# Optimization experiments

Hardware: AMD Instinct MI355X
Metric: run time of the kernel (lower is better)

Reference implementation:

```python
import jax, jax.numpy as jnp
import numpy as np

VJ = 80      # vjointnum (groups)
FS = 480     # feature_size = 2*k of RFF
HD = 256     # hidden_dim
K = 240      # RFF k
BATCH = 2048
TWO_PI = 2.0 * np.pi
SLOPE = 0.01  # LeakyReLU default negative_slope


def _wn(v, g):
    # weight_norm (dim=0): w[o,:] = g[o] * v[o,:] / ||v[o,:]||
    return v * (g[:, None] / jnp.linalg.norm(v, axis=1, keepdims=True))


def _grouped(x, v, g, b):
    # x: [B, G, in_g]; v: [G*out_g, in_g]; equivalent to groups=G Conv1d with kernel 1
    w = _wn(v, g)
    out_g = w.shape[0] // VJ
    y = jnp.einsum('bgi,goi->bgo', x, w.reshape(VJ, out_g, -1))
    return y + b.reshape(VJ, out_g)


def _lrelu(t):
    return jnp.where(t >= 0, t, SLOPE * t)


def setup_inputs() -> dict:
    key = jax.random.key(0)
    ks = jax.random.split(key, 12)
    d = {
        'querypoint': jax.random.normal(ks[0], (BATCH, VJ, 3), jnp.float32),
        'point_features': jax.random.normal(ks[1], (BATCH, VJ, FS), jnp.float32),
        'B_rff': jax.random.normal(ks[2], (3, K), jnp.float32),  # std=1
    }
    # per-group layer sizes: 480->512, 512->512, 512->256, 256->6
    dims = [(FS, 2 * HD), (2 * HD, 2 * HD), (2 * HD, HD), (HD, 6)]
    for i, (din, dout) in enumerate(dims):
        d[f'v{i}'] = jax.random.normal(ks[3 + 2 * i], (VJ * dout, din), jnp.float32) * 0.02
        d[f'g{i}'] = jnp.ones((VJ * dout,), jnp.float32)
        d[f'b{i}'] = jnp.zeros((VJ * dout,), jnp.float32)
    return d


def reference(querypoint, point_features, B_rff,
              v0, g0, b0, v1, g1, b1, v2, g2, b2, v3, g3, b3):
    # RFF encode: [B, N, 480]
    emb = TWO_PI * jnp.einsum('bnd,dk->bnk', querypoint, B_rff)
    feat = jnp.concatenate([jnp.cos(emb), jnp.sin(emb)], axis=-1)
    x = point_features + feat                       # [B, 80, 480]
    Bsz = x.shape[0]
    # transpose(-2,-1) then reshape(B, C*N, 1) with groups=80 ==> [B, 80, 480]
    x = jnp.transpose(x, (0, 2, 1)).reshape(Bsz, VJ, FS)
    x = _lrelu(_grouped(x, v0, g0, b0))             # [B, 80, 512]
    x = _lrelu(_grouped(x, v1, g1, b1))             # [B, 80, 512]
    x = _lrelu(_grouped(x, v2, g2, b2))             # [B, 80, 256]
    y = _grouped(x, v3, g3, b3)                     # [B, 80, 6]
    return y.reshape(Bsz, VJ, 6)
```

## Files before the change

kernel.cpp:

```cpp
#include <hip/hip_runtime.h>


typedef __attribute__((ext_vector_type(8)))  short short8;
typedef __attribute__((ext_vector_type(4)))  float f32x4;
typedef __attribute__((ext_vector_type(16))) float f32x16;
typedef __attribute__((ext_vector_type(4)))  unsigned short ushort4v;
typedef __attribute__((ext_vector_type(2)))  unsigned int uint2v;

#define VJ    80
#define FS    480
#define HD2   512
#define HD    256
#define BATCH 2048
#define SMLP  520

static __device__ __forceinline__ unsigned short f2bf(float f) {
  unsigned int u = __builtin_bit_cast(unsigned int, f);
  u += 0x7FFFu + ((u >> 16) & 1u);
  return (unsigned short)(u >> 16);
}

template<int K, int RPG>
static __device__ __forceinline__ void wfrag32_body(
    int blk, const float* __restrict__ v, const float* __restrict__ gain,
    unsigned short* __restrict__ dst, float* sV, float* sScale) {
  constexpr int KS = K / 16;
  constexpr int KP = K + 4;
  const int t  = threadIdx.x;
  const int n0 = blk * 32;
  const int g  = n0 / RPG;
  const int nt = (n0 % RPG) >> 5;

  const f32x4* v4 = (const f32x4*)(v + (size_t)n0 * K);
  for (int idx = t; idx < 32 * K / 4; idx += 512) {
    int row = idx / (K / 4), rem = idx - row * (K / 4);
    *(f32x4*)&sV[row * KP + rem * 4] = v4[idx];
  }
  __syncthreads();

  const int wave = t >> 6, lane = t & 63;
  for (int r = wave; r < 32; r += 8) {
    float s = 0.f;
    for (int k = lane; k < K; k += 64) { float x = sV[r * KP + k]; s += x * x; }
    #pragma unroll
    for (int off = 32; off > 0; off >>= 1) s += __shfl_down(s, off);
    if (lane == 0) sScale[r] = gain[n0 + r] / sqrtf(s);
  }
  __syncthreads();

  unsigned short* db = dst + (size_t)g * RPG * K + (size_t)nt * KS * 512;
  for (int o = t; o < KS * 64; o += 512) {
    int ks = o >> 6, l = o & 63;
    int nl = l & 31, k0 = ks * 16 + ((l >> 5) << 3);
    float sc = sScale[nl];
    short8 pk;
    #pragma unroll
    for (int j = 0; j < 8; ++j) pk[j] = (short)f2bf(sV[nl * KP + k0 + j] * sc);
    *(short8*)&db[(size_t)ks * 512 + l * 8] = pk;
  }
}

static __device__ __forceinline__ void w3frag_body(
    int gidx, const float* __restrict__ v3, const float* __restrict__ g3,
    unsigned short* __restrict__ W3f, float* sV, float* sScale) {
  const int t = threadIdx.x;
  const f32x4* v4 = (const f32x4*)(v3 + (size_t)gidx * 6 * 256);
  if (t < 384) {
    int row = t >> 6, rem = t & 63;
    *(f32x4*)&sV[row * 260 + rem * 4] = v4[t];
  }
  __syncthreads();
  const int wave = t >> 6, lane = t & 63;
  if (wave < 6) {
    float s = 0.f;
    #pragma unroll
    for (int k = 0; k < 4; ++k) { float x = sV[wave * 260 + lane + k * 64]; s += x * x; }
    #pragma unroll
    for (int off = 32; off > 0; off >>= 1) s += __shfl_down(s, off);
    if (lane == 0) sScale[wave] = g3[gidx * 6 + wave] / sqrtf(s);
  }
  __syncthreads();
  {
    int ks = t >> 6, l = t & 63;
    int c = l & 15, k0 = ks * 32 + ((l >> 4) << 3);
    short8 pk;
    #pragma unroll
    for (int j = 0; j < 8; ++j)
      pk[j] = (c < 6) ? (short)f2bf(sV[c * 260 + k0 + j] * sScale[c]) : (short)0;
    *(short8*)&W3f[(size_t)gidx * 4096 + (size_t)ks * 512 + l * 8] = pk;
  }
}

__global__ void __launch_bounds__(512)
prep_weights(const float* __restrict__ v0, const float* __restrict__ g0,
             const float* __restrict__ v1, const float* __restrict__ g1,
             const float* __restrict__ v2, const float* __restrict__ g2,
             const float* __restrict__ v3, const float* __restrict__ g3,
             unsigned short* __restrict__ W0, unsigned short* __restrict__ W1,
             unsigned short* __restrict__ W2, unsigned short* __restrict__ W3f) {
  __shared__ float sV[32 * 516];
  __shared__ float sScale[32];
  const int b = blockIdx.x;
  if      (b < 1280) wfrag32_body<480, 512>(b,        v0, g0, W0, sV, sScale);
  else if (b < 2560) wfrag32_body<512, 512>(b - 1280, v1, g1, W1, sV, sScale);
  else if (b < 3200) wfrag32_body<512, 256>(b - 2560, v2, g2, W2, sV, sScale);
  else               w3frag_body(b - 3200, v3, g3, W3f, sV, sScale);
}

__global__ void __launch_bounds__(1024)
prep_x(const float* __restrict__ qp, const float* __restrict__ pf,
       const float* __restrict__ Brff, unsigned short* __restrict__ Xg) {
  __shared__ float sB[720];
  __shared__ float sQ[240];
  __shared__ unsigned short sX[480 * 82];
  const int b = blockIdx.x;
  const int t = threadIdx.x;
  if (t < 720) sB[t] = Brff[t];
  if (t < 240) sQ[t] = qp[(size_t)b * 240 + t];
  __syncthreads();
  const float* pfb = pf + (size_t)b * 38400;
  #pragma unroll 2
  for (int idx = t; idx < 19200; idx += 1024) {
    int n2 = idx / 480;
    int c  = idx - n2 * 480;
    int n  = n2 * 2;
    int k  = (c < 240) ? c : c - 240;
    float bx = sB[k], by = sB[240 + k], bz = sB[480 + k];
    float d0 = sQ[n*3]   * bx + sQ[n*3+1] * by + sQ[n*3+2] * bz;
    float d1 = sQ[n*3+3] * bx + sQ[n*3+4] * by + sQ[n*3+5] * bz;
    float f0 = (c < 240) ? __builtin_amdgcn_cosf(d0) : __builtin_amdgcn_sinf(d0);
    float f1 = (c < 240) ? __builtin_amdgcn_cosf(d1) : __builtin_amdgcn_sinf(d1);
    unsigned int w = (unsigned int)f2bf(pfb[n * 480 + c] + f0)
                   | ((unsigned int)f2bf(pfb[(n + 1) * 480 + c] + f1) << 16);
    *(unsigned int*)&sX[c * 82 + n] = w;
  }
  __syncthreads();
  for (int idx4 = t; idx4 < 9600; idx4 += 1024) {
    int g  = idx4 / 120;
    int i4 = idx4 - g * 120;
    int i  = i4 * 4;
    int cl = i / 80;
    int n  = i - cl * 80;
    const unsigned int* p = (const unsigned int*)&sX[(g * 6 + cl) * 82 + n];
    uint2v val = { p[0], p[1] };
    *(uint2v*)(Xg + ((size_t)g * BATCH + b) * 480 + i) = val;
  }
}

#define MLP_STEP32(ksv, BB)                                                   \
  {                                                                           \
    const int ksc = (ksv);                                                    \
    short8 a0 = *(const short8*)(aB + ksc * 16);                              \
    short8 a1 = *(const short8*)(aB + 32 * SMLP + ksc * 16);                  \
           \
    short8 p0, p1;                                                            \
    const bool pf_ok = (ksc + 3 < KS);                                        \
    if (pf_ok) {                                                              \
      p0 = *(const short8*)(wB + ((size_t)0 * KS + ksc + 3) * 512);           \
      if (NT > 1) p1 = *(const short8*)(wB + ((size_t)1 * KS + ksc + 3) * 512); \
    }                                                                         \
    __builtin_amdgcn_s_setprio(1);                                            \
    _Pragma("unroll")                                                         \
    for (int nt = 0; nt < NT; ++nt)                                           \
      acc[0][nt] = __builtin_amdgcn_mfma_f32_32x32x16_bf16(a0, BB[nt], acc[0][nt], 0, 0, 0); \
    _Pragma("unroll")                                                         \
    for (int nt = 0; nt < NT; ++nt)                                           \
      acc[1][nt] = __builtin_amdgcn_mfma_f32_32x32x16_bf16(a1, BB[nt], acc[1][nt], 0, 0, 0); \
    __builtin_amdgcn_s_setprio(0);                                            \
    if (pf_ok) {                                                              \
      BB[0] = p0;                                                             \
      if (NT > 1) BB[1] = p1;                                                 \
    }                                                                         \
  }

template<int K, int N, bool ACT>
static __device__ __forceinline__ void run_layer32(
    unsigned short* __restrict__ s,
    const unsigned short* __restrict__ Wf, const float* __restrict__ bias,
    int wn, int lane) {
  constexpr int NT = N / 256;
  constexpr int KS = K / 16;
  const int nbase = wn * (N / 8);
  const int lr = lane & 31, lh = lane >> 5;

  f32x16 acc[2][NT];
  #pragma unroll
  for (int mt = 0; mt < 2; ++mt)
    #pragma unroll
    for (int nt = 0; nt < NT; ++nt)
      #pragma unroll
      for (int r = 0; r < 16; ++r) acc[mt][nt][r] = 0.f;

  const unsigned short* aB = s + lr * SMLP + lh * 8;
  const unsigned short* wB = Wf + (size_t)(wn * NT) * KS * 512 + lane * 8;

  short8 bb0[NT], bb1[NT], bb2[NT];
  #pragma unroll
  for (int nt = 0; nt < NT; ++nt) bb0[nt] = *(const short8*)(wB + ((size_t)nt * KS    ) * 512);
  #pragma unroll
  for (int nt = 0; nt < NT; ++nt) bb1[nt] = *(const short8*)(wB + ((size_t)nt * KS + 1) * 512);
  #pragma unroll
  for (int nt = 0; nt < NT; ++nt) bb2[nt] = *(const short8*)(wB + ((size_t)nt * KS + 2) * 512);

  #pragma unroll
  for (int ks3 = 0; ks3 < KS / 3; ++ks3) {
    MLP_STEP32(3 * ks3,     bb0);
    MLP_STEP32(3 * ks3 + 1, bb1);
    MLP_STEP32(3 * ks3 + 2, bb2);
  }
  if (KS % 3 == 2) {
    MLP_STEP32(KS - 2, bb0);
    MLP_STEP32(KS - 1, bb1);
  }

  float bv[NT];
  #pragma unroll
  for (int nt = 0; nt < NT; ++nt) bv[nt] = bias[nbase + nt * 32 + lr];

  __syncthreads();
  #pragma unroll
  for (int mt = 0; mt < 2; ++mt)
    #pragma unroll
    for (int nt = 0; nt < NT; ++nt)
      #pragma unroll
      for (int r = 0; r < 16; ++r) {
        float val = acc[mt][nt][r] + bv[nt];
        if (ACT) val = (val >= 0.f) ? val : 0.01f * val;
        const int row = mt * 32 + (r & 3) + 8 * (r >> 2) + 4 * lh;
        s[row * SMLP + (nbase + nt * 32 + lr)] = f2bf(val);
      }
  __syncthreads();
}

__global__ void __launch_bounds__(512, 4)
mlp_kernel(const unsigned short* __restrict__ Xg,
           const unsigned short* __restrict__ W0, const unsigned short* __restrict__ W1,
           const unsigned short* __restrict__ W2, const unsigned short* __restrict__ W3f,
           const float* __restrict__ b0, const float* __restrict__ b1,
           const float* __restrict__ b2, const float* __restrict__ b3,
           float* __restrict__ out) {
  __shared__ unsigned short s[64 * SMLP];

  const int bid   = blockIdx.x;
  const int xcd   = bid & 7;
  const int local = bid >> 3;
  const int g     = xcd * 10 + (local >> 5);
  const int tile  = local & 31;
  const int m0    = tile * 64;

  const int tid  = threadIdx.x, lane = tid & 63;
  const int wn   = tid >> 6;

  const unsigned short* Xs = Xg + ((size_t)g * BATCH + m0) * 480;
  for (int idx = tid; idx < 64 * 60; idx += 512) {
    int row = idx / 60, c = idx - row * 60;
    *(short8*)&s[row * SMLP + c * 8] = *(const short8*)(Xs + (size_t)row * 480 + c * 8);
  }
  __syncthreads();

  run_layer32<480, 512, true>(s, W0 + (size_t)g * 512 * 480, b0 + g * 512, wn, lane);
  run_layer32<512, 512, true>(s, W1 + (size_t)g * 512 * 512, b1 + g * 512, wn, lane);
  run_layer32<512, 256, true>(s, W2 + (size_t)g * 256 * 512, b2 + g * 256, wn, lane);

  if (wn < 4) {
    const int lr = lane & 15, lh = lane >> 4;
    const unsigned short* aB4 = s + (wn * 16 + lr) * SMLP + lh * 8;
    const unsigned short* w3  = W3f + (size_t)g * 4096 + lane * 8;
    f32x4 a4 = (f32x4){0.f, 0.f, 0.f, 0.f};
    #pragma unroll
    for (int kk = 0; kk < 8; ++kk) {
      short8 av  = *(const short8*)(aB4 + kk * 32);
      short8 wv8 = *(const short8*)(w3 + (size_t)kk * 512);
      a4 = __builtin_amdgcn_mfma_f32_16x16x32_bf16(av, wv8, a4, 0, 0, 0);
    }
    const int col = lane & 15;
    if (col < 6) {
      const float bias3 = b3[g * 6 + col];
      #pragma unroll
      for (int r = 0; r < 4; ++r)
        out[((size_t)(m0 + wn * 16 + lh * 4 + r) * VJ + g) * 6 + col] = a4[r] + bias3;
    }
  }
}

extern "C" void kernel_launch(void* const* d_in, const int* in_sizes, int n_in,
                              void* d_out, int out_size, void* d_ws, size_t ws_size,
                              hipStream_t stream) {
  const float* qp   = (const float*)d_in[0];
  const float* pf   = (const float*)d_in[1];
  const float* Brff = (const float*)d_in[2];
  const float* v0 = (const float*)d_in[3];  const float* g0 = (const float*)d_in[4];  const float* b0 = (const float*)d_in[5];
  const float* v1 = (const float*)d_in[6];  const float* g1 = (const float*)d_in[7];  const float* b1 = (const float*)d_in[8];
  const float* v2 = (const float*)d_in[9];  const float* g2 = (const float*)d_in[10]; const float* b2 = (const float*)d_in[11];
  const float* v3 = (const float*)d_in[12]; const float* g3 = (const float*)d_in[13]; const float* b3 = (const float*)d_in[14];

  unsigned short* W0  = (unsigned short*)d_ws;
  unsigned short* W1  = W0 + (size_t)VJ * HD2 * FS;
  unsigned short* W2  = W1 + (size_t)VJ * HD2 * HD2;
  unsigned short* W3f = W2 + (size_t)VJ * HD  * HD2;
  unsigned short* Xg  = W3f + (size_t)VJ * 4096;

  prep_weights<<<dim3(3280), dim3(512), 0, stream>>>(v0, g0, v1, g1, v2, g2, v3, g3,
                                                     W0, W1, W2, W3f);
  prep_x<<<dim3(BATCH), dim3(1024), 0, stream>>>(qp, pf, Brff, Xg);
  mlp_kernel<<<dim3(VJ * 32), dim3(512), 0, stream>>>(Xg, W0, W1, W2, W3f,
                                                      b0, b1, b2, b3, (float*)d_out);
}
```

Measured before the change: 401.9 us.

## Fuse RFF encoding and input transpose into MLP kernel prologue

Removes the separate prep_x kernel and its bf16 intermediate buffer. Each MLP block now computes the RFF cos/sin features, adds point_features and writes the transposed bf16 tile straight into shared memory. This saves one launch and a write and re-read of the intermediate tensor. In exchange, the gathers from pf are strided (6 floats per 480-float row), so global loads coalesce poorly, and the transcendental work is spread across the MLP blocks.

```diff
diff --git a/kernel.cpp b/kernel.cpp
--- a/kernel.cpp
+++ b/kernel.cpp
@@ -4,8 +4,6 @@
 typedef __attribute__((ext_vector_type(8)))  short short8;
 typedef __attribute__((ext_vector_type(4)))  float f32x4;
 typedef __attribute__((ext_vector_type(16))) float f32x16;
-typedef __attribute__((ext_vector_type(4)))  unsigned short ushort4v;
-typedef __attribute__((ext_vector_type(2)))  unsigned int uint2v;
 
 #define VJ    80
 #define FS    480
@@ -107,52 +105,11 @@
   else               w3frag_body(b - 3200, v3, g3, W3f, sV, sScale);
 }
 
-__global__ void __launch_bounds__(1024)
-prep_x(const float* __restrict__ qp, const float* __restrict__ pf,
-       const float* __restrict__ Brff, unsigned short* __restrict__ Xg) {
-  __shared__ float sB[720];
-  __shared__ float sQ[240];
-  __shared__ unsigned short sX[480 * 82];
-  const int b = blockIdx.x;
-  const int t = threadIdx.x;
-  if (t < 720) sB[t] = Brff[t];
-  if (t < 240) sQ[t] = qp[(size_t)b * 240 + t];
-  __syncthreads();
-  const float* pfb = pf + (size_t)b * 38400;
-  #pragma unroll 2
-  for (int idx = t; idx < 19200; idx += 1024) {
-    int n2 = idx / 480;
-    int c  = idx - n2 * 480;
-    int n  = n2 * 2;
-    int k  = (c < 240) ? c : c - 240;
-    float bx = sB[k], by = sB[240 + k], bz = sB[480 + k];
-    float d0 = sQ[n*3]   * bx + sQ[n*3+1] * by + sQ[n*3+2] * bz;
-    float d1 = sQ[n*3+3] * bx + sQ[n*3+4] * by + sQ[n*3+5] * bz;
-    float f0 = (c < 240) ? __builtin_amdgcn_cosf(d0) : __builtin_amdgcn_sinf(d0);
-    float f1 = (c < 240) ? __builtin_amdgcn_cosf(d1) : __builtin_amdgcn_sinf(d1);
-    unsigned int w = (unsigned int)f2bf(pfb[n * 480 + c] + f0)
-                   | ((unsigned int)f2bf(pfb[(n + 1) * 480 + c] + f1) << 16);
-    *(unsigned int*)&sX[c * 82 + n] = w;
-  }
-  __syncthreads();
-  for (int idx4 = t; idx4 < 9600; idx4 += 1024) {
-    int g  = idx4 / 120;
-    int i4 = idx4 - g * 120;
-    int i  = i4 * 4;
-    int cl = i / 80;
-    int n  = i - cl * 80;
-    const unsigned int* p = (const unsigned int*)&sX[(g * 6 + cl) * 82 + n];
-    uint2v val = { p[0], p[1] };
-    *(uint2v*)(Xg + ((size_t)g * BATCH + b) * 480 + i) = val;
-  }
-}
-
 #define MLP_STEP32(ksv, BB)                                                   \
   {                                                                           \
     const int ksc = (ksv);                                                    \
     short8 a0 = *(const short8*)(aB + ksc * 16);                              \
     short8 a1 = *(const short8*)(aB + 32 * SMLP + ksc * 16);                  \
-           \
     short8 p0, p1;                                                            \
     const bool pf_ok = (ksc + 3 < KS);                                        \
     if (pf_ok) {                                                              \
@@ -233,7 +190,8 @@
 }
 
 __global__ void __launch_bounds__(512, 4)
-mlp_kernel(const unsigned short* __restrict__ Xg,
+mlp_kernel(const float* __restrict__ qp, const float* __restrict__ pf,
+           const float* __restrict__ Brff,
            const unsigned short* __restrict__ W0, const unsigned short* __restrict__ W1,
            const unsigned short* __restrict__ W2, const unsigned short* __restrict__ W3f,
            const float* __restrict__ b0, const float* __restrict__ b1,
@@ -251,10 +209,30 @@
   const int tid  = threadIdx.x, lane = tid & 63;
   const int wn   = tid >> 6;
 
-  const unsigned short* Xs = Xg + ((size_t)g * BATCH + m0) * 480;
-  for (int idx = tid; idx < 64 * 60; idx += 512) {
-    int row = idx / 60, c = idx - row * 60;
-    *(short8*)&s[row * SMLP + c * 8] = *(const short8*)(Xs + (size_t)row * 480 + c * 8);
+  {
+    const int kbase = (g < 40) ? g * 6 : g * 6 - 240;
+    const bool ucos = (g < 40);
+    float Bx[6], By[6], Bz[6];
+    #pragma unroll
+    for (int j = 0; j < 6; ++j) {
+      Bx[j] = Brff[kbase + j];
+      By[j] = Brff[240 + kbase + j];
+      Bz[j] = Brff[480 + kbase + j];
+    }
+    for (int p = tid; p < 64 * 80; p += 512) {
+      int r = p / 80, n = p - r * 80;
+      const size_t brow = (size_t)(m0 + r);
+      const float* qpp = qp + brow * 240 + n * 3;
+      const float qx = qpp[0], qy = qpp[1], qz = qpp[2];
+      const float* pfp = pf + (brow * 80 + n) * 480 + g * 6;
+      unsigned short* sr = s + r * SMLP + n;
+      #pragma unroll
+      for (int j = 0; j < 6; ++j) {
+        float d = qx * Bx[j] + qy * By[j] + qz * Bz[j];
+        float f = ucos ? __builtin_amdgcn_cosf(d) : __builtin_amdgcn_sinf(d);
+        sr[j * 80] = f2bf(pfp[j] + f);
+      }
+    }
   }
   __syncthreads();
 
@@ -298,11 +276,9 @@
   unsigned short* W1  = W0 + (size_t)VJ * HD2 * FS;
   unsigned short* W2  = W1 + (size_t)VJ * HD2 * HD2;
   unsigned short* W3f = W2 + (size_t)VJ * HD  * HD2;
-  unsigned short* Xg  = W3f + (size_t)VJ * 4096;
 
   prep_weights<<<dim3(3280), dim3(512), 0, stream>>>(v0, g0, v1, g1, v2, g2, v3, g3,
                                                      W0, W1, W2, W3f);
-  prep_x<<<dim3(BATCH), dim3(1024), 0, stream>>>(qp, pf, Brff, Xg);
-  mlp_kernel<<<dim3(VJ * 32), dim3(512), 0, stream>>>(Xg, W0, W1, W2, W3f,
+  mlp_kernel<<<dim3(VJ * 32), dim3(512), 0, stream>>>(qp, pf, Brff, W0, W1, W2, W3f,
                                                       b0, b1, b2, b3, (float*)d_out);
 }
```

After: 449.8 us. +11.9%, slower.
